# Optimization experiments

Measured on AMD Instinct MI355X. Metric: run time of the kernel, lower is better.

## Reference

```python
import jax, jax.numpy as jnp
import numpy as np

# task -> non-background class ids, padded with -1 to fixed width 3
NBG = np.array([[0, 1, 2], [0, 3, 4], [0, 5, 6], [0, 7, 8],
                [0, 9, -1], [0, 10, -1], [0, 11, -1]], dtype=np.int32)
NEG = -1e9      # pad logit (finite stand-in for -inf, grad-safe)
SMOOTH = 1e-5
NUM_CLASSES = 12


def setup_inputs() -> dict:
    key = jax.random.key(0)
    k1, k2, k3 = jax.random.split(key, 3)
    B, C, D, H, W = 4, 12, 32, 128, 128
    inputs = jax.random.normal(k1, (B, C, D, H, W), dtype=jnp.float32)
    task_id = jax.random.randint(k2, (B,), 0, 7, dtype=jnp.int32)
    # build targets consistent with each sample's task: labels in task_nbg[task]
    raw = jax.random.randint(k3, (B, D, H, W), 0, 3, dtype=jnp.int32)
    nbg = jnp.asarray(NBG)
    ids = nbg[task_id]                                   # [B,3]
    valid_max = jnp.where(ids[:, 2] < 0, 1, 2)           # 2-class tasks: raw in {0,1}
    raw = jnp.minimum(raw, valid_max[:, None, None, None])
    targets = jnp.take_along_axis(ids, raw.reshape(B, -1), axis=1).reshape(B, D, H, W)
    return {"inputs": inputs, "targets": targets, "task_id": task_id}


def reference(inputs, targets, task_id):
    B = inputs.shape[0]
    probs = jax.nn.softmax(inputs, axis=1)               # [B,12,D,H,W]
    nbg = jnp.asarray(NBG)
    ids = nbg[task_id]                                   # [B,3]
    mask = (ids >= 0)                                    # [B,3]
    idsc = jnp.maximum(ids, 0)
    mask5 = mask[:, :, None, None, None]
    gathered = jnp.take_along_axis(probs, idsc[:, :, None, None, None], axis=1)  # [B,3,D,H,W]
    score = jnp.where(mask5, gathered, 0.0)

    # --- remapped marginal targets: labels > 0 shifted by delta ---
    t = task_id.astype(jnp.int32)
    delta = jnp.where(t <= 4, -2 * t, -t - 4)
    tm = jnp.where(targets > 0, targets + delta[:, None, None, None], targets)   # in {0,1,2}

    # --- marginal CE: log_softmax over gathered probs (note: probs, not logits, matching torch F.cross_entropy on softmaxed inputs) ---
    logits = jnp.where(mask5, gathered, NEG)
    logp = jax.nn.log_softmax(logits, axis=1)
    nll = -jnp.take_along_axis(logp, tm[:, None], axis=1)[:, 0]                  # [B,D,H,W]
    loss_marg_ce = nll.mean(axis=(1, 2, 3)).sum() / B

    # --- marginal dice (padded classes contribute exactly 0) ---
    tgt = ((targets[:, None] == idsc[:, :, None, None, None]) & mask5).astype(probs.dtype)
    inter = jnp.sum(score * tgt, axis=(2, 3, 4))
    y_sum = jnp.sum(tgt, axis=(2, 3, 4))                 # tgt is binary: tgt*tgt == tgt
    z_sum = jnp.sum(score * score, axis=(2, 3, 4))
    dice = (2 * inter + SMOOTH) / (z_sum + y_sum + SMOOTH)
    loss_marg_dice = (1.0 - dice).sum() / B

    # --- exclusion: target_e = 1 - onehot(targets, 0..11), class 0 zeroed ---
    cls = jnp.arange(NUM_CLASSES, dtype=targets.dtype)[None, :, None, None, None]
    onehot = (targets[:, None] == cls).astype(probs.dtype)
    te = 1.0 - onehot
    te = te.at[:, 0].set(0.0)
    inter_e = jnp.sum(probs * te, axis=(2, 3, 4))
    y_e = jnp.sum(te, axis=(2, 3, 4))
    z_e = jnp.sum(probs * probs, axis=(2, 3, 4))
    dice_e = (2 * inter_e + SMOOTH) / (z_e + y_e + SMOOTH)
    loss_exc_dice = dice_e.sum() / B                     # inv=True: sum of dice scores

    loss_exc_ce = (jnp.log1p(probs) * te).mean(axis=(2, 3, 4)).sum() / B

    return (loss_marg_dice, loss_marg_ce, loss_exc_dice, loss_exc_ce)
```

## Files before the change

### kernel.cpp

```cpp
#include <hip/hip_runtime.h>


#define S4 131072
#define BLOCKS_PER_B 128
#define THREADS 256
#define NVOX 524288.0f
#define SMOOTH 1e-5f

#define WRED(v) { v += __shfl_down(v,32); v += __shfl_down(v,16); \
                  v += __shfl_down(v,8);  v += __shfl_down(v,4);  \
                  v += __shfl_down(v,2);  v += __shfl_down(v,1); }

#define PROC(COMP) do {                                                        \
  float xv[12];                                                                \
  _Pragma("unroll")                                                            \
  for (int c = 0; c < 12; ++c) xv[c] = x[c].COMP;                              \
  const int tgt = tg.COMP;                                                     \
  float m = xv[0];                                                             \
  _Pragma("unroll")                                                            \
  for (int c = 1; c < 12; ++c) m = fmaxf(m, xv[c]);                            \
  float e[12]; float es = 0.f;                                                 \
  _Pragma("unroll")                                                            \
  for (int c = 0; c < 12; ++c) { e[c] = __expf(xv[c] - m); es += e[c]; }       \
  const float r = 1.0f / es;                                                   \
  float g0 = 0.f, g1 = 0.f, g2 = 0.f;                                          \
  _Pragma("unroll")                                                            \
  for (int c = 0; c < 12; ++c) {                                               \
    const float p = e[c] * r;                                                  \
    aZ[c] += p * p;                                                            \
    const bool isT = (tgt == c);                                               \
    aC[c] += isT ? 1.f : 0.f;                                                  \
    if (c > 0) {                                                               \
      aIE[c] += isT ? 0.f : p;                                                 \
      aCE[c] += isT ? 0.f : __logf(1.f + p);                                   \
    }                                                                          \
    if (c == 0) g0 = p;                                                        \
    if (c==1||c==3||c==5||c==7||c==9||c==10||c==11) g1 = (id1==c) ? p : g1;    \
    if (c==2||c==4||c==6||c==8)                     g2 = (id2==c) ? p : g2;    \
  }                                                                            \
  const float s2v = v2 ? g2 : 0.f;                                             \
  zm0 += g0*g0; zm1 += g1*g1; zm2 += s2v*s2v;                                  \
  const bool t0 = (tgt == 0);                                                  \
  const bool t1 = (tgt == id1);                                                \
  const bool t2 = v2 && (tgt == id2);                                          \
  im0 += t0 ? g0 : 0.f; im1 += t1 ? g1 : 0.f; im2 += t2 ? g2 : 0.f;            \
  float m3 = fmaxf(g0, g1);                                                    \
  if (v2) m3 = fmaxf(m3, g2);                                                  \
  float s3 = __expf(g0 - m3) + __expf(g1 - m3);                                \
  if (v2) s3 += __expf(g2 - m3);                                               \
  const float lse = m3 + __logf(s3);                                           \
  const float gt = t0 ? g0 : (t1 ? g1 : g2);                                   \
  ces += lse - gt;                                                             \
} while (0)

__global__ void zero_acc(float* __restrict__ acc) {
  acc[threadIdx.x] = 0.f;
}

__global__ __launch_bounds__(THREADS, 2)
void marg_main(const float4* __restrict__ inp, const int4* __restrict__ tgtp,
               const int* __restrict__ task_id, float* __restrict__ acc) {
  const int b   = blockIdx.x >> 7;
  const int blk = blockIdx.x & (BLOCKS_PER_B - 1);
  const int t   = task_id[b];
  const int id1 = (t <= 4) ? 2*t + 1 : t + 5;
  const int id2 = (t <= 3) ? 2*t + 2 : -1;
  const bool v2 = (id2 >= 0);

  const float4* inB = inp  + (size_t)b * 12 * S4;
  const int4*   tgB = tgtp + (size_t)b * S4;

  float aZ[12], aIE[12], aCE[12], aC[12];
  #pragma unroll
  for (int c = 0; c < 12; ++c) { aZ[c]=0.f; aIE[c]=0.f; aCE[c]=0.f; aC[c]=0.f; }
  float zm0=0.f, zm1=0.f, zm2=0.f, im0=0.f, im1=0.f, im2=0.f, ces=0.f;

  #pragma unroll 1
  for (int s = blk * THREADS + (int)threadIdx.x; s < S4; s += BLOCKS_PER_B * THREADS) {
    float4 x[12];
    #pragma unroll
    for (int c = 0; c < 12; ++c) x[c] = inB[c * S4 + s];
    const int4 tg = tgB[s];
    PROC(x); PROC(y); PROC(z); PROC(w);
  }

  WRED(ces); WRED(im0); WRED(im1); WRED(im2); WRED(zm0); WRED(zm1); WRED(zm2);
  #pragma unroll
  for (int c = 0; c < 12; ++c) { WRED(aZ[c]); WRED(aIE[c]); WRED(aCE[c]); WRED(aC[c]); }

  __shared__ float red[4][64];
  const int lane = threadIdx.x & 63;
  const int wv   = threadIdx.x >> 6;
  if (lane == 0) {
    float* rw = red[wv];
    rw[0]=ces; rw[1]=im0; rw[2]=im1; rw[3]=im2; rw[4]=zm0; rw[5]=zm1; rw[6]=zm2; rw[7]=0.f;
    #pragma unroll
    for (int c = 0; c < 12; ++c) {
      rw[8+c]=aZ[c]; rw[20+c]=aIE[c]; rw[32+c]=aCE[c]; rw[44+c]=aC[c];
    }
  }
  __syncthreads();
  if (threadIdx.x < 56) {
    const float sv = red[0][threadIdx.x] + red[1][threadIdx.x]
                   + red[2][threadIdx.x] + red[3][threadIdx.x];
    atomicAdd(acc + b * 64 + threadIdx.x, sv);
  }
}

__global__ void finalize(const float* __restrict__ acc,
                         const int* __restrict__ task_id,
                         float* __restrict__ out) {
  if (threadIdx.x != 0) return;
  float lmd = 0.f, lmce = 0.f, led = 0.f, lece = 0.f;
  for (int b = 0; b < 4; ++b) {
    const float* a = acc + b * 64;
    const int t   = task_id[b];
    const int id1 = (t <= 4) ? 2*t + 1 : t + 5;
    const int id2 = (t <= 3) ? 2*t + 2 : -1;

    lmce += a[0] / NVOX;

    const float y0 = a[44 + 0];
    const float y1 = a[44 + id1];
    const float d0 = (2.f*a[1] + SMOOTH) / (a[4] + y0 + SMOOTH);
    const float d1 = (2.f*a[2] + SMOOTH) / (a[5] + y1 + SMOOTH);
    float d2 = 1.f;
    if (id2 >= 0) {
      const float y2 = a[44 + id2];
      d2 = (2.f*a[3] + SMOOTH) / (a[6] + y2 + SMOOTH);
    }
    lmd += (1.f - d0) + (1.f - d1) + (1.f - d2);

    led += SMOOTH / (a[8] + SMOOTH);
    for (int c = 1; c < 12; ++c) {
      const float ye = NVOX - a[44 + c];
      led += (2.f*a[20 + c] + SMOOTH) / (a[8 + c] + ye + SMOOTH);
    }

    float s = 0.f;
    for (int c = 1; c < 12; ++c) s += a[32 + c];
    lece += s / NVOX;
  }
  out[0] = lmd  * 0.25f;
  out[1] = lmce * 0.25f;
  out[2] = led  * 0.25f;
  out[3] = lece * 0.25f;
}

extern "C" void kernel_launch(void* const* d_in, const int* in_sizes, int n_in,
                              void* d_out, int out_size, void* d_ws, size_t ws_size,
                              hipStream_t stream) {
  const float* inputs  = (const float*)d_in[0];
  const int*   targets = (const int*)d_in[1];
  const int*   task_id = (const int*)d_in[2];
  float* out = (float*)d_out;
  float* acc = (float*)d_ws;

  zero_acc<<<1, 256, 0, stream>>>(acc);
  marg_main<<<dim3(4 * BLOCKS_PER_B), THREADS, 0, stream>>>(
      (const float4*)inputs, (const int4*)targets, task_id, acc);
  finalize<<<1, 64, 0, stream>>>(acc, task_id, out);
}
```

Before: 170.0 us.

## Exploit target structure to shrink accumulators and raise occupancy

Targets only ever hold class 0, id1 or id2, so the per-class exclusion sums are rebuilt in finalize from total probability sums minus the matched-target terms. This cuts per-thread accumulators from 48+7 to 24+8. Per-voxel log1p is summed unconditionally, with the target term subtracted afterwards. Launch bounds rise to 4 waves per SIMD and the grid doubles to 256 blocks per batch with a fixed two-iteration loop. The rewrite assumes targets are always one of the task's classes and may lose float precision in the subtraction.

```diff
diff --git a/kernel.cpp b/kernel.cpp
--- a/kernel.cpp
+++ b/kernel.cpp
@@ -2,7 +2,7 @@
 
 
 #define S4 131072
-#define BLOCKS_PER_B 128
+#define BLOCKS_PER_B 256
 #define THREADS 256
 #define NVOX 524288.0f
 #define SMOOTH 1e-5f
@@ -22,28 +22,31 @@
   float e[12]; float es = 0.f;                                                 \
   _Pragma("unroll")                                                            \
   for (int c = 0; c < 12; ++c) { e[c] = __expf(xv[c] - m); es += e[c]; }       \
-  const float r = 1.0f / es;                                                   \
-  float g0 = 0.f, g1 = 0.f, g2 = 0.f;                                          \
+  const float r = __builtin_amdgcn_rcpf(es);                                   \
+  float p[12];                                                                 \
   _Pragma("unroll")                                                            \
   for (int c = 0; c < 12; ++c) {                                               \
-    const float p = e[c] * r;                                                  \
-    aZ[c] += p * p;                                                            \
-    const bool isT = (tgt == c);                                               \
-    aC[c] += isT ? 1.f : 0.f;                                                  \
-    if (c > 0) {                                                               \
-      aIE[c] += isT ? 0.f : p;                                                 \
-      aCE[c] += isT ? 0.f : __logf(1.f + p);                                   \
-    }                                                                          \
-    if (c == 0) g0 = p;                                                        \
-    if (c==1||c==3||c==5||c==7||c==9||c==10||c==11) g1 = (id1==c) ? p : g1;    \
-    if (c==2||c==4||c==6||c==8)                     g2 = (id2==c) ? p : g2;    \
+    p[c] = e[c] * r;                                                           \
+    aZ[c] += p[c] * p[c];                                                      \
+    aP[c] += p[c];                                                             \
   }                                                                            \
-  const float s2v = v2 ? g2 : 0.f;                                             \
-  zm0 += g0*g0; zm1 += g1*g1; zm2 += s2v*s2v;                                  \
+  float slog = 0.f;                                                            \
+  _Pragma("unroll")                                                            \
+  for (int c = 1; c < 12; ++c) slog += __logf(1.f + p[c]);                     \
+  const float g0 = p[0];                                                       \
+  float g1 = 0.f, g2 = 0.f;                                                    \
+  _Pragma("unroll")                                                            \
+  for (int c = 1; c < 12; ++c) {                                               \
+    if (c==1||c==3||c==5||c==7||c==9||c==10||c==11) g1 = (id1==c) ? p[c] : g1; \
+    else                                            g2 = (id2==c) ? p[c] : g2; \
+  }                                                                            \
   const bool t0 = (tgt == 0);                                                  \
   const bool t1 = (tgt == id1);                                                \
   const bool t2 = v2 && (tgt == id2);                                          \
-  im0 += t0 ? g0 : 0.f; im1 += t1 ? g1 : 0.f; im2 += t2 ? g2 : 0.f;            \
+  c0 += t0 ? 1.f : 0.f;  c1 += t1 ? 1.f : 0.f;  c2 += t2 ? 1.f : 0.f;          \
+  p0S += t0 ? g0 : 0.f;  p1S += t1 ? g1 : 0.f;  p2S += t2 ? g2 : 0.f;          \
+  const float pt = t1 ? g1 : (t2 ? g2 : 0.f);                                  \
+  cesE += slog - __logf(1.f + pt);                                             \
   float m3 = fmaxf(g0, g1);                                                    \
   if (v2) m3 = fmaxf(m3, g2);                                                  \
   float s3 = __expf(g0 - m3) + __expf(g1 - m3);                                \
@@ -57,11 +60,11 @@
   acc[threadIdx.x] = 0.f;
 }
 
-__global__ __launch_bounds__(THREADS, 2)
+__global__ __launch_bounds__(THREADS, 4)
 void marg_main(const float4* __restrict__ inp, const int4* __restrict__ tgtp,
                const int* __restrict__ task_id, float* __restrict__ acc) {
-  const int b   = blockIdx.x >> 7;
-  const int blk = blockIdx.x & (BLOCKS_PER_B - 1);
+  const int b   = blockIdx.x / BLOCKS_PER_B;
+  const int blk = blockIdx.x % BLOCKS_PER_B;
   const int t   = task_id[b];
   const int id1 = (t <= 4) ? 2*t + 1 : t + 5;
   const int id2 = (t <= 3) ? 2*t + 2 : -1;
@@ -70,13 +73,14 @@
   const float4* inB = inp  + (size_t)b * 12 * S4;
   const int4*   tgB = tgtp + (size_t)b * S4;
 
-  float aZ[12], aIE[12], aCE[12], aC[12];
+  float aZ[12], aP[12];
   #pragma unroll
-  for (int c = 0; c < 12; ++c) { aZ[c]=0.f; aIE[c]=0.f; aCE[c]=0.f; aC[c]=0.f; }
-  float zm0=0.f, zm1=0.f, zm2=0.f, im0=0.f, im1=0.f, im2=0.f, ces=0.f;
+  for (int c = 0; c < 12; ++c) { aZ[c]=0.f; aP[c]=0.f; }
+  float ces=0.f, cesE=0.f, c0=0.f, c1=0.f, c2=0.f, p0S=0.f, p1S=0.f, p2S=0.f;
 
   #pragma unroll 1
-  for (int s = blk * THREADS + (int)threadIdx.x; s < S4; s += BLOCKS_PER_B * THREADS) {
+  for (int it = 0; it < 2; ++it) {
+    const int s = (blk * 2 + it) * THREADS + (int)threadIdx.x;
     float4 x[12];
     #pragma unroll
     for (int c = 0; c < 12; ++c) x[c] = inB[c * S4 + s];
@@ -84,23 +88,23 @@
     PROC(x); PROC(y); PROC(z); PROC(w);
   }
 
-  WRED(ces); WRED(im0); WRED(im1); WRED(im2); WRED(zm0); WRED(zm1); WRED(zm2);
+  WRED(ces); WRED(cesE); WRED(c0); WRED(c1); WRED(c2);
+  WRED(p0S); WRED(p1S); WRED(p2S);
   #pragma unroll
-  for (int c = 0; c < 12; ++c) { WRED(aZ[c]); WRED(aIE[c]); WRED(aCE[c]); WRED(aC[c]); }
+  for (int c = 0; c < 12; ++c) { WRED(aZ[c]); WRED(aP[c]); }
 
-  __shared__ float red[4][64];
+  __shared__ float red[4][32];
   const int lane = threadIdx.x & 63;
   const int wv   = threadIdx.x >> 6;
   if (lane == 0) {
     float* rw = red[wv];
-    rw[0]=ces; rw[1]=im0; rw[2]=im1; rw[3]=im2; rw[4]=zm0; rw[5]=zm1; rw[6]=zm2; rw[7]=0.f;
+    rw[0]=ces; rw[1]=cesE; rw[2]=c0; rw[3]=c1; rw[4]=c2;
+    rw[5]=p0S; rw[6]=p1S; rw[7]=p2S;
     #pragma unroll
-    for (int c = 0; c < 12; ++c) {
-      rw[8+c]=aZ[c]; rw[20+c]=aIE[c]; rw[32+c]=aCE[c]; rw[44+c]=aC[c];
-    }
+    for (int c = 0; c < 12; ++c) { rw[8+c]=aZ[c]; rw[20+c]=aP[c]; }
   }
   __syncthreads();
-  if (threadIdx.x < 56) {
+  if (threadIdx.x < 32) {
     const float sv = red[0][threadIdx.x] + red[1][threadIdx.x]
                    + red[2][threadIdx.x] + red[3][threadIdx.x];
     atomicAdd(acc + b * 64 + threadIdx.x, sv);
@@ -119,27 +123,23 @@
     const int id2 = (t <= 3) ? 2*t + 2 : -1;
 
     lmce += a[0] / NVOX;
+    lece += a[1] / NVOX;
 
-    const float y0 = a[44 + 0];
-    const float y1 = a[44 + id1];
-    const float d0 = (2.f*a[1] + SMOOTH) / (a[4] + y0 + SMOOTH);
-    const float d1 = (2.f*a[2] + SMOOTH) / (a[5] + y1 + SMOOTH);
+    const float d0 = (2.f*a[5] + SMOOTH) / (a[8 + 0]   + a[2] + SMOOTH);
+    const float d1 = (2.f*a[6] + SMOOTH) / (a[8 + id1] + a[3] + SMOOTH);
     float d2 = 1.f;
-    if (id2 >= 0) {
-      const float y2 = a[44 + id2];
-      d2 = (2.f*a[3] + SMOOTH) / (a[6] + y2 + SMOOTH);
-    }
+    if (id2 >= 0)
+      d2 = (2.f*a[7] + SMOOTH) / (a[8 + id2] + a[4] + SMOOTH);
     lmd += (1.f - d0) + (1.f - d1) + (1.f - d2);
 
     led += SMOOTH / (a[8] + SMOOTH);
     for (int c = 1; c < 12; ++c) {
-      const float ye = NVOX - a[44 + c];
-      led += (2.f*a[20 + c] + SMOOTH) / (a[8 + c] + ye + SMOOTH);
+      const float ptc  = (c == id1) ? a[6] : ((c == id2) ? a[7] : 0.f);
+      const float cntc = (c == id1) ? a[3] : ((c == id2) ? a[4] : 0.f);
+      const float inter = a[20 + c] - ptc;
+      const float ye    = NVOX - cntc;
+      led += (2.f*inter + SMOOTH) / (a[8 + c] + ye + SMOOTH);
     }
-
-    float s = 0.f;
-    for (int c = 1; c < 12; ++c) s += a[32 + c];
-    lece += s / NVOX;
   }
   out[0] = lmd  * 0.25f;
   out[1] = lmce * 0.25f;
```

Result: no change. 167.2 us (-1.7%).
